# Kernel tuning notes

Measured on AMD Instinct MI355X. Metric: run time of the kernel, lower is better.

The kernel has to match this reference:

```python
import jax, jax.numpy as jnp
import numpy as np

RADIUS = 1.0
NSAMPLE = 32


def _query_ball(new_xyz, xyz, radius, nsample):
    # new_xyz (B,M,3), xyz (B,N,3) -> idx (B,M,nsample) int32
    B, M, _ = new_xyz.shape
    N = xyz.shape[1]
    # squared distances via ||q||^2 + ||p||^2 - 2 q.p (avoids BxMxNx3 diff tensor)
    q2 = jnp.sum(new_xyz * new_xyz, axis=-1)          # (B,M)
    p2 = jnp.sum(xyz * xyz, axis=-1)                  # (B,N)
    qp = jnp.einsum('bmd,bnd->bmn', new_xyz, xyz)     # (B,M,N)
    dist2 = q2[:, :, None] + p2[:, None, :] - 2.0 * qp
    mask = dist2 < radius * radius
    ar = jnp.arange(N, dtype=jnp.int32)
    masked = jnp.where(mask, ar[None, None, :], jnp.int32(N + 1))  # (B,M,N)
    first = jnp.sort(masked, axis=2)[:, :, :nsample]               # (B,M,S)
    first_valid = first[:, :, :1]                                   # pad with first neighbor
    idx = jnp.where(first == N + 1, first_valid, first)
    return idx.astype(jnp.int32)


def _group(points, idx):
    # points (B,C,N), idx (B,M,S) -> (B,C,M,S) gather along N
    B, C, N = points.shape
    M, S = idx.shape[1], idx.shape[2]
    ie = jnp.broadcast_to(idx.reshape(B, 1, M * S).astype(jnp.int32), (B, C, M * S))
    return jnp.take_along_axis(points, ie, axis=2).reshape(B, C, M, S)


def setup_inputs() -> dict:
    key = jax.random.key(0)
    k1, k2 = jax.random.split(key)
    B, N, M, C = 8, 8192, 2048, 64
    xyz = jax.random.normal(k1, (B, N, 3), dtype=jnp.float32)
    # centroids are a subset of the cloud -> every ball query has >= 1 valid neighbor
    new_xyz = xyz[:, :M, :]
    features = jax.random.normal(k2, (B, C, N), dtype=jnp.float32)
    return {"xyz": xyz, "new_xyz": new_xyz, "features": features}


def reference(xyz, new_xyz, features):
    idx = _query_ball(new_xyz, xyz, RADIUS, NSAMPLE)                      # (B,M,S)
    grouped_xyz = _group(jnp.swapaxes(xyz, 1, 2), idx)                    # (B,3,M,S)
    grouped_xyz = grouped_xyz - jnp.swapaxes(new_xyz, 1, 2)[..., None]    # recenter
    grouped_feat = _group(features, idx)                                  # (B,C,M,S)
    return jnp.concatenate([grouped_xyz, grouped_feat], axis=1)           # (B,3+C,M,S)
```

## Files before the change

### kernel.cpp

```cpp
#include <hip/hip_runtime.h>

#define N_PTS 8192
#define M_Q   2048
#define C_F   64
#define NS    32
#define B_SZ  8

__global__ __launch_bounds__(256) void prep_kernel(
    const float* __restrict__ feat, const float* __restrict__ xyz,
    float* __restrict__ featT, float4* __restrict__ xyz4)
{
#pragma clang fp contract(off)
    __shared__ float lds[C_F * 65];
    if (blockIdx.x < B_SZ * 128) {
        const int b  = blockIdx.x >> 7;
        const int n0 = (blockIdx.x & 127) * 64;
        {
            const int c4 = threadIdx.x >> 6;
            const int nn = threadIdx.x & 63;
#pragma unroll
            for (int k = 0; k < 16; ++k) {
                const int c = k * 4 + c4;
                lds[c * 65 + nn] = feat[((size_t)b * C_F + c) * N_PTS + n0 + nn];
            }
        }
        __syncthreads();
        {
            const int n4 = threadIdx.x >> 6;
            const int c  = threadIdx.x & 63;
#pragma unroll
            for (int k = 0; k < 16; ++k) {
                const int nn = k * 4 + n4;
                featT[((size_t)b * N_PTS + n0 + nn) * C_F + c] = lds[c * 65 + nn];
            }
        }
    } else {
        const int i = (blockIdx.x - B_SZ * 128) * 256 + (int)threadIdx.x;
        const float p0 = xyz[i * 3 + 0];
        const float p1 = xyz[i * 3 + 1];
        const float p2 = xyz[i * 3 + 2];
        const float s  = (p0 * p0 + p1 * p1) + p2 * p2;
        xyz4[i] = make_float4(p0, p1, p2, s);
    }
}

__global__ __launch_bounds__(256) void qbg_kernel(
    const float4* __restrict__ xyz4, const float* __restrict__ nxyz,
    const float* __restrict__ featT, float* __restrict__ out)
{
#pragma clang fp contract(off)
    __shared__ int   sidx[4][NS];
    __shared__ float stage[67 * 33];

    const int lane = threadIdx.x & 63;
    const int w    = threadIdx.x >> 6;
    const int q    = blockIdx.x * 4 + w;
    const int b    = q >> 11;
    const float4* __restrict__ xb = xyz4 + (size_t)b * N_PTS;

    {
        const float* __restrict__ qp = nxyz + (size_t)q * 3;
        const float qx = qp[0], qy = qp[1], qz = qp[2];
        const float q2 = (qx * qx + qy * qy) + qz * qz;

        int  cnt = 0;
        int  first_idx = 0;
        bool have_first = false;

        for (int base = 0; base < N_PTS && cnt < NS; base += 256) {
            float4 P[4];
#pragma unroll
            for (int cc = 0; cc < 4; ++cc)
                P[cc] = xb[base + cc * 64 + lane];
#pragma unroll
            for (int cc = 0; cc < 4; ++cc) {
                if (cnt >= NS) break;
                const float qpdot = (qx * P[cc].x + qy * P[cc].y) + qz * P[cc].z;
                const float d2 = (q2 + P[cc].w) - 2.0f * qpdot;
                const bool pred = d2 < 1.0f;
                const unsigned long long mask = __ballot(pred);
                if (mask) {
                    if (!have_first) {
                        first_idx = base + cc * 64 + __ffsll(mask) - 1;
                        have_first = true;
                    }
                    if (pred) {
                        const int pos = cnt + (int)__popcll(mask & ((1ull << lane) - 1ull));
                        if (pos < NS) sidx[w][pos] = base + cc * 64 + lane;
                    }
                    cnt += (int)__popcll(mask);
                }
            }
        }
        if (cnt < NS) {
            for (int p = cnt + lane; p < NS; p += 64) sidx[w][p] = first_idx;
        }
    }
    __syncthreads();

    const int pS = threadIdx.x >> 3;
    const int j  = threadIdx.x & 7;
    const size_t cstride = (size_t)M_Q * NS;

    for (int w2 = 0; w2 < 4; ++w2) {
        const int qq = blockIdx.x * 4 + w2;
        const int mm = qq & (M_Q - 1);
        const int n  = sidx[w2][pS];

        const float* __restrict__ fb = featT + ((size_t)b * N_PTS + n) * C_F;
#pragma unroll
        for (int k = 0; k < 2; ++k) {
            const int c = k * 32 + j * 4;
            const float4 v = *(const float4*)(fb + c);
            stage[(3 + c + 0) * 33 + pS] = v.x;
            stage[(3 + c + 1) * 33 + pS] = v.y;
            stage[(3 + c + 2) * 33 + pS] = v.z;
            stage[(3 + c + 3) * 33 + pS] = v.w;
        }
        if (j == 0) {
            const float4 pv = xb[n];
            const float* __restrict__ qp2 = nxyz + (size_t)qq * 3;
            stage[0 * 33 + pS] = pv.x - qp2[0];
            stage[1 * 33 + pS] = pv.y - qp2[1];
            stage[2 * 33 + pS] = pv.z - qp2[2];
        }
        __syncthreads();

        const size_t obase = ((size_t)b * 67 * M_Q + mm) * NS;
#pragma unroll
        for (int it = 0; it < 3; ++it) {
            const int e = it * 256 + (int)threadIdx.x;
            if (e < 67 * 8) {
                const int row  = e >> 3;
                const int col4 = (e & 7) * 4;
                float4 v;
                v.x = stage[row * 33 + col4 + 0];
                v.y = stage[row * 33 + col4 + 1];
                v.z = stage[row * 33 + col4 + 2];
                v.w = stage[row * 33 + col4 + 3];
                *(float4*)&out[obase + (size_t)row * cstride + col4] = v;
            }
        }
        __syncthreads();
    }
}

extern "C" void kernel_launch(void* const* d_in, const int* in_sizes, int n_in,
                              void* d_out, int out_size, void* d_ws, size_t ws_size,
                              hipStream_t stream)
{
    const float* xyz  = (const float*)d_in[0];
    const float* nxyz = (const float*)d_in[1];
    const float* feat = (const float*)d_in[2];
    float* out = (float*)d_out;

    float*  featT = (float*)d_ws;
    float4* xyz4  = (float4*)((char*)d_ws + (20 << 20));

    const int Q = B_SZ * M_Q;

    prep_kernel<<<B_SZ * 128 + (B_SZ * N_PTS) / 256, 256, 0, stream>>>(
        feat, xyz, featT, xyz4);
    qbg_kernel<<<Q / 4, 256, 0, stream>>>(xyz4, nxyz, featT, out);
}
```

Measured before the change: 178.5 us.

## Prefetch next point chunk and write grouped output directly without LDS staging

The ball-query scan now software-prefetches the next 256 points into registers while testing the current chunk, to hide global load latency. The gather phase drops the LDS transpose stage and its two block barriers per query. Instead, each thread loads 16 contiguous features for one sample and writes them straight to the output as scalar stores, coalesced across the 32 samples. This trades float4 stores for more, narrower stores but removes the LDS traffic and synchronisation. It also processes two queries per iteration.

```diff
diff --git a/kernel.cpp b/kernel.cpp
--- a/kernel.cpp
+++ b/kernel.cpp
@@ -49,8 +49,7 @@
     const float* __restrict__ featT, float* __restrict__ out)
 {
 #pragma clang fp contract(off)
-    __shared__ int   sidx[4][NS];
-    __shared__ float stage[67 * 33];
+    __shared__ int sidx[4][NS];
 
     const int lane = threadIdx.x & 63;
     const int w    = threadIdx.x >> 6;
@@ -67,11 +66,16 @@
         int  first_idx = 0;
         bool have_first = false;
 
+        float4 P[4], Pn[4];
+#pragma unroll
+        for (int cc = 0; cc < 4; ++cc) P[cc] = xb[cc * 64 + lane];
+
         for (int base = 0; base < N_PTS && cnt < NS; base += 256) {
-            float4 P[4];
+            const int nb = base + 256;
+            if (nb < N_PTS) {
 #pragma unroll
-            for (int cc = 0; cc < 4; ++cc)
-                P[cc] = xb[base + cc * 64 + lane];
+                for (int cc = 0; cc < 4; ++cc) Pn[cc] = xb[nb + cc * 64 + lane];
+            }
 #pragma unroll
             for (int cc = 0; cc < 4; ++cc) {
                 if (cnt >= NS) break;
@@ -91,6 +95,8 @@
                     cnt += (int)__popcll(mask);
                 }
             }
+#pragma unroll
+            for (int cc = 0; cc < 4; ++cc) P[cc] = Pn[cc];
         }
         if (cnt < NS) {
             for (int p = cnt + lane; p < NS; p += 64) sidx[w][p] = first_idx;
@@ -98,50 +104,40 @@
     }
     __syncthreads();
 
-    const int pS = threadIdx.x >> 3;
-    const int j  = threadIdx.x & 7;
+    const int j  = threadIdx.x & 3;
+    const int s  = (threadIdx.x >> 2) & 31;
+    const int qs = threadIdx.x >> 7;
     const size_t cstride = (size_t)M_Q * NS;
 
-    for (int w2 = 0; w2 < 4; ++w2) {
-        const int qq = blockIdx.x * 4 + w2;
-        const int mm = qq & (M_Q - 1);
-        const int n  = sidx[w2][pS];
+    for (int g = 0; g < 2; ++g) {
+        const int widx = g * 2 + qs;
+        const int qq   = blockIdx.x * 4 + widx;
+        const int mm   = qq & (M_Q - 1);
+        const int n    = sidx[widx][s];
 
-        const float* __restrict__ fb = featT + ((size_t)b * N_PTS + n) * C_F;
+        const float* __restrict__ fb =
+            featT + ((size_t)b * N_PTS + n) * C_F + j * 16;
+        const float4 v0 = ((const float4*)fb)[0];
+        const float4 v1 = ((const float4*)fb)[1];
+        const float4 v2 = ((const float4*)fb)[2];
+        const float4 v3 = ((const float4*)fb)[3];
+        const float f[16] = { v0.x, v0.y, v0.z, v0.w,  v1.x, v1.y, v1.z, v1.w,
+                              v2.x, v2.y, v2.z, v2.w,  v3.x, v3.y, v3.z, v3.w };
+
+        const size_t obase = ((size_t)b * 67 * M_Q + mm) * NS + s;
+        float* __restrict__ op = out + obase + (size_t)(3 + j * 16) * cstride;
 #pragma unroll
-        for (int k = 0; k < 2; ++k) {
-            const int c = k * 32 + j * 4;
-            const float4 v = *(const float4*)(fb + c);
-            stage[(3 + c + 0) * 33 + pS] = v.x;
-            stage[(3 + c + 1) * 33 + pS] = v.y;
-            stage[(3 + c + 2) * 33 + pS] = v.z;
-            stage[(3 + c + 3) * 33 + pS] = v.w;
-        }
+        for (int i = 0; i < 16; ++i)
+            op[(size_t)i * cstride] = f[i];
+
         if (j == 0) {
             const float4 pv = xb[n];
             const float* __restrict__ qp2 = nxyz + (size_t)qq * 3;
-            stage[0 * 33 + pS] = pv.x - qp2[0];
-            stage[1 * 33 + pS] = pv.y - qp2[1];
-            stage[2 * 33 + pS] = pv.z - qp2[2];
+            float* __restrict__ ox = out + obase;
+            ox[0]           = pv.x - qp2[0];
+            ox[cstride]     = pv.y - qp2[1];
+            ox[2 * cstride] = pv.z - qp2[2];
         }
-        __syncthreads();
-
-        const size_t obase = ((size_t)b * 67 * M_Q + mm) * NS;
-#pragma unroll
-        for (int it = 0; it < 3; ++it) {
-            const int e = it * 256 + (int)threadIdx.x;
-            if (e < 67 * 8) {
-                const int row  = e >> 3;
-                const int col4 = (e & 7) * 4;
-                float4 v;
-                v.x = stage[row * 33 + col4 + 0];
-                v.y = stage[row * 33 + col4 + 1];
-                v.z = stage[row * 33 + col4 + 2];
-                v.w = stage[row * 33 + col4 + 3];
-                *(float4*)&out[obase + (size_t)row * cstride + col4] = v;
-            }
-        }
-        __syncthreads();
     }
 }
 
```

Result: slower. 187.4 us (+5.0%).

## Stage all four queries' gathered rows at once and write contiguous 512B output runs

Applied to the files above, without the earlier changes.

The gather/transpose phase now stages all 4 queries of a block (128 samples) into one larger LDS tile with a single barrier, instead of looping over queries with two barriers each. Because the block's queries are consecutive in M, each output row segment becomes 128 contiguous floats, giving longer coalesced stores. It also issues all feature gathers up front for more memory-level parallelism. The cost is larger LDS use (about 36KB), which may reduce occupancy, and LDS bank conflicts are possible with the 133 stride.

```diff
diff --git a/kernel.cpp b/kernel.cpp
--- a/kernel.cpp
+++ b/kernel.cpp
@@ -50,7 +50,7 @@
 {
 #pragma clang fp contract(off)
     __shared__ int   sidx[4][NS];
-    __shared__ float stage[67 * 33];
+    __shared__ float st[67][133];
 
     const int lane = threadIdx.x & 63;
     const int w    = threadIdx.x >> 6;
@@ -98,50 +98,55 @@
     }
     __syncthreads();
 
-    const int pS = threadIdx.x >> 3;
-    const int j  = threadIdx.x & 7;
-    const size_t cstride = (size_t)M_Q * NS;
+    {
+        const int c4  = threadIdx.x & 15;
+        const int spl = threadIdx.x >> 4;
+        const float4* __restrict__ fT =
+            (const float4*)(featT + (size_t)b * N_PTS * C_F);
+#pragma unroll
+        for (int loop = 0; loop < 8; ++loop) {
+            const int sp = loop * 16 + spl;
+            const int ql = sp >> 5;
+            const int s  = sp & 31;
+            const int n  = sidx[ql][s];
+            const float4 v = fT[(size_t)n * 16 + c4];
+            st[3 + c4 * 4 + 0][sp] = v.x;
+            st[3 + c4 * 4 + 1][sp] = v.y;
+            st[3 + c4 * 4 + 2][sp] = v.z;
+            st[3 + c4 * 4 + 3][sp] = v.w;
+        }
+        if (threadIdx.x < 128) {
+            const int sp = threadIdx.x;
+            const int ql = sp >> 5;
+            const int s  = sp & 31;
+            const int qq = blockIdx.x * 4 + ql;
+            const int n  = sidx[ql][s];
+            const float4 pv = xb[n];
+            st[0][sp] = pv.x - nxyz[qq * 3 + 0];
+            st[1][sp] = pv.y - nxyz[qq * 3 + 1];
+            st[2][sp] = pv.z - nxyz[qq * 3 + 2];
+        }
+    }
+    __syncthreads();
 
-    for (int w2 = 0; w2 < 4; ++w2) {
-        const int qq = blockIdx.x * 4 + w2;
-        const int mm = qq & (M_Q - 1);
-        const int n  = sidx[w2][pS];
-
-        const float* __restrict__ fb = featT + ((size_t)b * N_PTS + n) * C_F;
+    {
+        const int m0 = (blockIdx.x * 4) & (M_Q - 1);
+        const size_t cstride = (size_t)M_Q * NS;
+        const size_t obase = (size_t)b * 67 * cstride + (size_t)m0 * NS;
 #pragma unroll
-        for (int k = 0; k < 2; ++k) {
-            const int c = k * 32 + j * 4;
-            const float4 v = *(const float4*)(fb + c);
-            stage[(3 + c + 0) * 33 + pS] = v.x;
-            stage[(3 + c + 1) * 33 + pS] = v.y;
-            stage[(3 + c + 2) * 33 + pS] = v.z;
-            stage[(3 + c + 3) * 33 + pS] = v.w;
-        }
-        if (j == 0) {
-            const float4 pv = xb[n];
-            const float* __restrict__ qp2 = nxyz + (size_t)qq * 3;
-            stage[0 * 33 + pS] = pv.x - qp2[0];
-            stage[1 * 33 + pS] = pv.y - qp2[1];
-            stage[2 * 33 + pS] = pv.z - qp2[2];
-        }
-        __syncthreads();
-
-        const size_t obase = ((size_t)b * 67 * M_Q + mm) * NS;
-#pragma unroll
-        for (int it = 0; it < 3; ++it) {
+        for (int it = 0; it < 9; ++it) {
             const int e = it * 256 + (int)threadIdx.x;
-            if (e < 67 * 8) {
-                const int row  = e >> 3;
-                const int col4 = (e & 7) * 4;
+            if (e < 67 * 32) {
+                const int row = e >> 5;
+                const int g   = e & 31;
                 float4 v;
-                v.x = stage[row * 33 + col4 + 0];
-                v.y = stage[row * 33 + col4 + 1];
-                v.z = stage[row * 33 + col4 + 2];
-                v.w = stage[row * 33 + col4 + 3];
-                *(float4*)&out[obase + (size_t)row * cstride + col4] = v;
+                v.x = st[row][g * 4 + 0];
+                v.y = st[row][g * 4 + 1];
+                v.z = st[row][g * 4 + 2];
+                v.w = st[row][g * 4 + 3];
+                *(float4*)&out[obase + (size_t)row * cstride + g * 4] = v;
             }
         }
-        __syncthreads();
     }
 }
 
```

Result: slower. 185.0 us (+3.6%).
